# Kernel tuning notes

Measured on AMD Instinct MI355X. Metric: run time of the kernel, lower is better.

## Reference

```python
import jax, jax.numpy as jnp
import numpy as np

B, C, H, W = 8, 256, 64, 64
NH, FF, L, K = 8, 1024, 3, 64
THR = 0.5
DH = C // NH
SCALE = 1.0 / float(np.sqrt(DH))
N = H * W


def setup_inputs() -> dict:
    key = jax.random.key(0)
    ks = jax.random.split(key, 16)
    s = 0.02
    rn = lambda k, shape: (jax.random.normal(k, shape, jnp.float32) * s)
    return {
        "x": jax.random.normal(ks[0], (B, C, H, W), jnp.float32),
        "y": jax.random.normal(ks[1], (B, C, H, W), jnp.float32),
        "proj_w": rn(ks[2], (C, 2 * C)), "proj_b": rn(ks[3], (C,)),
        "sal_w": rn(ks[4], (1, C)), "sal_b": rn(ks[5], (1,)),
        "soft_w": rn(ks[6], (2, K, C)), "soft_b": rn(ks[7], (2, K)),
        "attn_in_w": rn(ks[8], (2, L, 3 * C, C)), "attn_in_b": rn(ks[9], (2, L, 3 * C)),
        "attn_out_w": rn(ks[10], (2, L, C, C)), "attn_out_b": rn(ks[11], (2, L, C)),
        "n1_g": jnp.ones((2, L, C), jnp.float32), "n1_b": jnp.zeros((2, L, C), jnp.float32),
        "ffn_w1": rn(ks[12], (2, L, FF, C)), "ffn_b1": rn(ks[13], (2, L, FF)),
        "ffn_w2": rn(ks[14], (2, L, C, FF)), "ffn_b2": rn(ks[15], (2, L, C)),
        "n2_g": jnp.ones((2, L, C), jnp.float32), "n2_b": jnp.zeros((2, L, C), jnp.float32),
    }


def _ln(t, g, b, eps=1e-5):
    m = t.mean(-1, keepdims=True)
    v = ((t - m) ** 2).mean(-1, keepdims=True)
    return (t - m) / jnp.sqrt(v + eps) * g + b


def _layers(q, kv, p, side):
    # q: [B,N,C] pixel queries, kv: [B,K,C] soft-pooled tokens
    for l in range(L):
        iw, ib = p["attn_in_w"][side, l], p["attn_in_b"][side, l]
        qq = (q @ iw[:C].T + ib[:C]).reshape(B, -1, NH, DH)
        kk = (kv @ iw[C:2 * C].T + ib[C:2 * C]).reshape(B, K, NH, DH)
        vv = (kv @ iw[2 * C:].T + ib[2 * C:]).reshape(B, K, NH, DH)
        att = jax.nn.softmax(jnp.einsum('bnhd,bkhd->bhnk', qq, kk) * SCALE, axis=-1)
        o = jnp.einsum('bhnk,bkhd->bnhd', att, vv).reshape(B, -1, C)
        o = o @ p["attn_out_w"][side, l].T + p["attn_out_b"][side, l]
        q = _ln(q + o, p["n1_g"][side, l], p["n1_b"][side, l])
        h = jax.nn.relu(q @ p["ffn_w1"][side, l].T + p["ffn_b1"][side, l])
        h = h @ p["ffn_w2"][side, l].T + p["ffn_b2"][side, l]
        q = _ln(q + h, p["n2_g"][side, l], p["n2_b"][side, l])
    return q


def _forward(x, y, proj_w, proj_b, sal_w, sal_b, soft_w, soft_b,
             attn_in_w, attn_in_b, attn_out_w, attn_out_b, n1_g, n1_b,
             ffn_w1, ffn_b1, ffn_w2, ffn_b2, n2_g, n2_b):
    p = dict(attn_in_w=attn_in_w, attn_in_b=attn_in_b, attn_out_w=attn_out_w,
             attn_out_b=attn_out_b, n1_g=n1_g, n1_b=n1_b, ffn_w1=ffn_w1,
             ffn_b1=ffn_b1, ffn_w2=ffn_w2, ffn_b2=ffn_b2, n2_g=n2_g, n2_b=n2_b)
    xc = jnp.concatenate([x, y], axis=1)                                  # [B,2C,H,W]
    feat = jnp.einsum('oc,bchw->bohw', proj_w, xc) + proj_b[None, :, None, None]
    sal = jnp.einsum('oc,bchw->bohw', sal_w, feat) + sal_b[None, :, None, None]  # [B,1,H,W]
    heat = jax.nn.sigmoid(sal)
    fg_mask = (heat >= THR).reshape(B, 1, N)
    bg_mask = (heat < 1.0 - THR).reshape(B, 1, N)
    fmap = feat.reshape(B, C, N)
    q0 = fmap.transpose(0, 2, 1)                                          # [B,N,C]
    out = fmap
    for side, hm in ((0, heat), (1, 1.0 - heat)):
        wf = feat * hm                                                    # [B,C,H,W]
        sw = (jnp.einsum('kc,bchw->bkhw', soft_w[side], wf)
              + soft_b[side][None, :, None, None]).reshape(B, K, N)       # [B,K,N]
        pool = jnp.einsum('bkn,bcn->bkc', sw, wf.reshape(B, C, N))        # [B,K,C]
        qs = _layers(q0, pool, p, side)                                   # [B,N,C]
        mask = fg_mask if side == 0 else bg_mask
        out = jnp.where(mask, qs.transpose(0, 2, 1), out)
    # per-image skip: if no fg or no bg pixels, keep original feature
    valid = fg_mask.any(axis=(1, 2)) & bg_mask.any(axis=(1, 2))           # [B]
    out = jnp.where(valid[:, None, None], out, fmap)
    return out.reshape(B, C, H, W)


def reference(x, y, proj_w, proj_b, sal_w, sal_b, soft_w, soft_b,
              attn_in_w, attn_in_b, attn_out_w, attn_out_b, n1_g, n1_b,
              ffn_w1, ffn_b1, ffn_w2, ffn_b2, n2_g, n2_b):
    return _forward(x, y, proj_w, proj_b, sal_w, sal_b, soft_w, soft_b,
                    attn_in_w, attn_in_b, attn_out_w, attn_out_b, n1_g, n1_b,
                    ffn_w1, ffn_b1, ffn_w2, ffn_b2, n2_g, n2_b)
```

## Files before the change

### kernel.cpp

```cpp
#include <hip/hip_runtime.h>
#include <stdint.h>

#define B_ 8
#define C_ 256
#define N_ 4096
#define K_ 64
#define NH_ 8
#define FF_ 1024
#define L_ 3
#define M_ (B_*N_)
#define SCALE_ 0.17677669529663687f

typedef float f32x4 __attribute__((ext_vector_type(4)));
typedef __bf16 v8bf __attribute__((ext_vector_type(8)));

__device__ __forceinline__ float b2f(unsigned short h){
  union { uint32_t u; float f; } v; v.u = ((uint32_t)h) << 16; return v.f;
}
__device__ __forceinline__ unsigned short f2b(float f){
  union { float f; uint32_t u; } v; v.f = f;
  uint32_t r = v.u + 0x7fffu + ((v.u >> 16) & 1u);
  return (unsigned short)(r >> 16);
}
__device__ __forceinline__ void gload_lds16(const void* g, void* l){
  __builtin_amdgcn_global_load_lds(
      (const __attribute__((address_space(1))) unsigned int*)g,
      (__attribute__((address_space(3))) unsigned int*)l, 16, 0, 0);
}

__global__ __launch_bounds__(256) void k_f32_to_bf16(const float* __restrict__ src,
                                                     unsigned short* __restrict__ dst, int n){
  int i4 = (blockIdx.x*256 + threadIdx.x)*4;
  if (i4 >= n) return;
  float4 v = *(const float4*)(src + i4);
  uint32_t p0 = (uint32_t)f2b(v.x) | ((uint32_t)f2b(v.y) << 16);
  uint32_t p1 = (uint32_t)f2b(v.z) | ((uint32_t)f2b(v.w) << 16);
  *(uint2*)(dst + i4) = make_uint2(p0, p1);
}

__global__ __launch_bounds__(256) void k_build_xcT(const float* __restrict__ x,
                                                   const float* __restrict__ y,
                                                   unsigned short* __restrict__ xcT){
  __shared__ float t[32][33];
  int b = blockIdx.z;
  int n0 = blockIdx.x*32, c0 = blockIdx.y*32;
  int tx = threadIdx.x, ty = threadIdx.y;
  const float* src = (c0 < 256) ? (x + ((size_t)b*256 + c0)*N_)
                                : (y + ((size_t)b*256 + (c0-256))*N_);
  #pragma unroll
  for (int i = 0; i < 4; i++){
    int cl = ty*4 + i;
    t[cl][tx] = src[(size_t)cl*N_ + n0 + tx];
  }
  __syncthreads();
  #pragma unroll
  for (int i = 0; i < 4; i++){
    int nl = ty*4 + i;
    xcT[((size_t)b*N_ + n0 + nl)*512 + c0 + tx] = f2b(t[tx][nl]);
  }
}

__global__ __launch_bounds__(256) void k_featmir(const float* __restrict__ featT,
                                                 unsigned short* __restrict__ featbf,
                                                 unsigned short* __restrict__ featC){
  __shared__ float t[32][33];
  int b = blockIdx.z;
  int n0 = blockIdx.x*32, c0 = blockIdx.y*32;
  int tx = threadIdx.x, ty = threadIdx.y;
  #pragma unroll
  for (int i = 0; i < 4; i++){
    int nl = ty*4 + i;
    size_t m = (size_t)b*N_ + n0 + nl;
    float v = featT[m*256 + c0 + tx];
    t[nl][tx] = v;
    featbf[m*256 + c0 + tx] = f2b(v);
  }
  __syncthreads();
  #pragma unroll
  for (int i = 0; i < 4; i++){
    int cl = ty*4 + i;
    featC[((size_t)b*256 + c0 + cl)*(size_t)N_ + n0 + tx] = f2b(t[tx][cl]);
  }
}

__global__ __launch_bounds__(512) void k_compute_u(const float* __restrict__ sal_w,
                                                   const float* __restrict__ proj_w,
                                                   const float* __restrict__ proj_b,
                                                   const float* __restrict__ sal_b,
                                                   double* __restrict__ u){
  int c2 = threadIdx.x;
  double acc = 0.0;
  for (int c = 0; c < 256; ++c)
    acc += (double)sal_w[c] * (double)proj_w[(size_t)c*512 + c2];
  u[c2] = acc;
  if (c2 == 0){
    double s0 = (double)sal_b[0];
    for (int c = 0; c < 256; ++c) s0 += (double)sal_w[c] * (double)proj_b[c];
    u[512] = s0;
  }
}

__global__ __launch_bounds__(256) void k_sal_part(const float* __restrict__ x,
                                                  const float* __restrict__ y,
                                                  const double* __restrict__ u,
                                                  double* __restrict__ part){
  int pix = blockIdx.x*256 + threadIdx.x;
  int cc = blockIdx.y;
  int b = pix >> 12, n = pix & 4095;
  int c0 = cc*32;
  const float* src = (c0 < 256) ? (x + ((size_t)b*256 + c0)*N_ + n)
                                : (y + ((size_t)b*256 + (c0-256))*N_ + n);
  const double* uu = u + c0;
  double acc = 0.0;
  #pragma unroll 8
  for (int c = 0; c < 32; ++c) acc += uu[c] * (double)src[(size_t)c*N_];
  part[(size_t)cc*32768 + pix] = acc;
}

__global__ __launch_bounds__(256) void k_sal_red(const double* __restrict__ part,
                                                 const double* __restrict__ u,
                                                 float* __restrict__ heat,
                                                 int* __restrict__ counts){
  int pix = blockIdx.x*256 + threadIdx.x;
  int b = pix >> 12;
  double acc = u[512];
  #pragma unroll
  for (int cc = 0; cc < 16; cc++) acc += part[(size_t)cc*32768 + pix];
  float hf = (float)(1.0 / (1.0 + exp(-acc)));
  heat[pix] = hf;
  unsigned long long mfg = __ballot(hf >= 0.5f);
  unsigned long long mbg = __ballot(hf < 0.5f);
  if ((threadIdx.x & 63) == 0){
    atomicAdd(&counts[b*2+0], (int)__popcll(mfg));
    atomicAdd(&counts[b*2+1], (int)__popcll(mbg));
  }
}

template<int EPI>
__global__ __launch_bounds__(256) void k_gemm_bt(
    const unsigned short* __restrict__ A, const unsigned short* __restrict__ W,
    const float* __restrict__ bias, void* __restrict__ out,
    int M, int N, int K){
  __shared__ unsigned short smem[2][2][128*64];
  int tid = threadIdx.x;
  int w = tid >> 6, l = tid & 63;
  int m0 = blockIdx.x * 128, n0 = blockIdx.y * 128;
  int wr = w >> 1, wc = w & 1;
  int lr = l & 15, lk = l >> 4;
  f32x4 acc[4][4] = {};
  int nt = K >> 6;
  #pragma unroll
  for (int i = 0; i < 4; i++){
    int idx = i*256 + tid;
    int row = idx >> 3, su = ((idx & 7) ^ (row & 7))*8;
    gload_lds16(A + (size_t)(m0+row)*K + su, &smem[0][0][idx*8]);
    gload_lds16(W + (size_t)(n0+row)*K + su, &smem[0][1][idx*8]);
  }
  __syncthreads();
  for (int t = 0; t < nt; ++t){
    int cur = t & 1;
    if (t + 1 < nt){
      int k0 = (t + 1) << 6;
      #pragma unroll
      for (int i = 0; i < 4; i++){
        int idx = i*256 + tid;
        int row = idx >> 3, su = ((idx & 7) ^ (row & 7))*8;
        gload_lds16(A + (size_t)(m0+row)*K + k0 + su, &smem[cur^1][0][idx*8]);
        gload_lds16(W + (size_t)(n0+row)*K + k0 + su, &smem[cur^1][1][idx*8]);
      }
    }
    const unsigned short* ldsA = smem[cur][0];
    const unsigned short* ldsB = smem[cur][1];
    #pragma unroll
    for (int kk = 0; kk < 2; kk++){
      v8bf af[4], bfr[4];
      #pragma unroll
      for (int f = 0; f < 4; f++){
        int ra = wr*64 + f*16 + lr;
        int rb2 = wc*64 + f*16 + lr;
        int u = kk*4 + lk;
        af[f]  = *(const v8bf*)(&ldsA[ra*64 + ((u ^ (ra&7))<<3)]);
        bfr[f] = *(const v8bf*)(&ldsB[rb2*64 + ((u ^ (rb2&7))<<3)]);
      }
      #pragma unroll
      for (int fi = 0; fi < 4; fi++)
        #pragma unroll
        for (int fj = 0; fj < 4; fj++)
          acc[fi][fj] = __builtin_amdgcn_mfma_f32_16x16x32_bf16(af[fi], bfr[fj], acc[fi][fj], 0, 0, 0);
    }
    __syncthreads();
  }
  if (EPI == 1 || EPI == 2){
    unsigned short* st = &smem[0][0][0];
    #pragma unroll
    for (int fj = 0; fj < 4; fj++){
      int col = wc*64 + fj*16 + lr;
      float bv = bias[n0 + col];
      #pragma unroll
      for (int fi = 0; fi < 4; fi++){
        int rl = wr*64 + fi*16 + lk*4;
        #pragma unroll
        for (int r = 0; r < 4; r++){
          float v = acc[fi][fj][r] + bv;
          if (EPI == 1) v = fmaxf(v, 0.f);
          st[(rl + r)*136 + col] = f2b(v);
        }
      }
    }
    __syncthreads();
    #pragma unroll
    for (int it = 0; it < 8; it++){
      int idx = it*256 + tid;
      int row = idx >> 4, c8 = (idx & 15)*8;
      *(uint4*)((unsigned short*)out + (size_t)(m0+row)*N + n0 + c8)
          = *(const uint4*)&st[row*136 + c8];
    }
  } else {
    #pragma unroll
    for (int fj = 0; fj < 4; fj++){
      int col = n0 + wc*64 + fj*16 + lr;
      float bv = bias[col];
      #pragma unroll
      for (int fi = 0; fi < 4; fi++){
        int rb = m0 + wr*64 + fi*16 + lk*4;
        #pragma unroll
        for (int r = 0; r < 4; r++){
          float v = acc[fi][fj][r] + bv;
          if (EPI == 3){
            int row = rb + r;
            ((unsigned short*)out)[((size_t)(row>>6)*256 + col)*64 + (row&63)] = f2b(v);
          } else {
            ((float*)out)[(size_t)(rb + r)*N + col] = v;
          }
        }
      }
    }
  }
}

__global__ __launch_bounds__(256) void k_kv(
    const unsigned short* __restrict__ pool, const unsigned short* __restrict__ iw,
    const float* __restrict__ ib, unsigned short* __restrict__ kk_bf,
    unsigned short* __restrict__ vvT_bf){
  __shared__ unsigned short smem[2][2][128*64];
  int tid = threadIdx.x;
  int w = tid >> 6, l = tid & 63;
  int m0 = blockIdx.x * 128, n0 = blockIdx.y * 128;
  int isv = blockIdx.z;
  const unsigned short* W = iw + (size_t)(isv ? 512 : 256)*256;
  const float* bias = ib + (isv ? 512 : 256);
  int wr = w >> 1, wc = w & 1;
  int lr = l & 15, lk = l >> 4;
  f32x4 acc[4][4] = {};
  #pragma unroll
  for (int i = 0; i < 4; i++){
    int idx = i*256 + tid;
    int row = idx >> 3, su = ((idx & 7) ^ (row & 7))*8;
    gload_lds16(pool + (size_t)(m0+row)*256 + su, &smem[0][0][idx*8]);
    gload_lds16(W + (size_t)(n0+row)*256 + su, &smem[0][1][idx*8]);
  }
  __syncthreads();
  for (int t = 0; t < 4; ++t){
    int cur = t & 1;
    if (t + 1 < 4){
      int k0 = (t + 1) << 6;
      #pragma unroll
      for (int i = 0; i < 4; i++){
        int idx = i*256 + tid;
        int row = idx >> 3, su = ((idx & 7) ^ (row & 7))*8;
        gload_lds16(pool + (size_t)(m0+row)*256 + k0 + su, &smem[cur^1][0][idx*8]);
        gload_lds16(W + (size_t)(n0+row)*256 + k0 + su, &smem[cur^1][1][idx*8]);
      }
    }
    const unsigned short* ldsA = smem[cur][0];
    const unsigned short* ldsB = smem[cur][1];
    #pragma unroll
    for (int kk = 0; kk < 2; kk++){
      v8bf af[4], bfr[4];
      #pragma unroll
      for (int f = 0; f < 4; f++){
        int ra = wr*64 + f*16 + lr;
        int rb2 = wc*64 + f*16 + lr;
        int u = kk*4 + lk;
        af[f]  = *(const v8bf*)(&ldsA[ra*64 + ((u ^ (ra&7))<<3)]);
        bfr[f] = *(const v8bf*)(&ldsB[rb2*64 + ((u ^ (rb2&7))<<3)]);
      }
      #pragma unroll
      for (int fi = 0; fi < 4; fi++)
        #pragma unroll
        for (int fj = 0; fj < 4; fj++)
          acc[fi][fj] = __builtin_amdgcn_mfma_f32_16x16x32_bf16(af[fi], bfr[fj], acc[fi][fj], 0, 0, 0);
    }
    __syncthreads();
  }
  #pragma unroll
  for (int fj = 0; fj < 4; fj++){
    int col = n0 + wc*64 + fj*16 + lr;
    float bv = bias[col];
    #pragma unroll
    for (int fi = 0; fi < 4; fi++){
      int rb = m0 + wr*64 + fi*16 + lk*4;
      #pragma unroll
      for (int r = 0; r < 4; r++){
        float v = acc[fi][fj][r] + bv;
        int row = rb + r;
        if (isv)
          vvT_bf[((size_t)(row>>6)*256 + col)*64 + (row&63)] = f2b(v);
        else
          kk_bf[(size_t)row*256 + col] = f2b(v);
      }
    }
  }
}

__global__ __launch_bounds__(512) void k_ffn(
    const unsigned short* __restrict__ qb, const unsigned short* __restrict__ W1g,
    const float* __restrict__ b1g, const unsigned short* __restrict__ W2g,
    const float* __restrict__ b2g, const float* __restrict__ n2g,
    const float* __restrict__ n2b, unsigned short* __restrict__ qout){
  __shared__ unsigned short smem[73728];
  unsigned short* sA  = smem;
  unsigned short* sW1 = smem + 32768;
  unsigned short* sW2 = smem + 49152;
  unsigned short* sH  = smem + 65536;
  int tid = threadIdx.x;
  int w = tid >> 6, l = tid & 63;
  int m0 = blockIdx.x * 128;
  int wm = w >> 2;
  int wf = w & 3;
  int lr = l & 15, lk = l >> 4;

  #pragma unroll
  for (int i = 0; i < 8; i++){
    int idx = i*512 + tid;
    int row = idx >> 5, g = idx & 31;
    int su = (g & 24) | ((g & 7) ^ (row & 7));
    gload_lds16(qb + (size_t)(m0+row)*256 + su*8, &sA[idx*8]);
  }
  #pragma unroll
  for (int i = 0; i < 4; i++){
    int idx = i*512 + tid;
    int row = idx >> 5, g = idx & 31;
    int su = (g & 24) | ((g & 7) ^ (row & 7));
    gload_lds16(W1g + (size_t)row*256 + su*8, &sW1[idx*8]);
  }
  #pragma unroll
  for (int i = 0; i < 4; i++){
    int idx = i*512 + tid;
    int row = idx >> 3, g = idx & 7;
    int su = g ^ (row & 7);
    gload_lds16(W2g + (size_t)row*1024 + su*8, &sW2[idx*8]);
  }
  __syncthreads();

  f32x4 acc[4][4] = {};
  for (int cc = 0; cc < 16; ++cc){
    f32x4 hacc[4] = {};
    #pragma unroll
    for (int ks = 0; ks < 8; ks++){
      int g = ks*4 + lk;
      int rf = wf*16 + lr;
      v8bf bf1 = *(const v8bf*)&sW1[rf*256 + (((g & 24) | ((g & 7) ^ (rf & 7)))<<3)];
      #pragma unroll
      for (int f = 0; f < 4; f++){
        int ra = wm*64 + f*16 + lr;
        v8bf af = *(const v8bf*)&sA[ra*256 + (((g & 24) | ((g & 7) ^ (ra & 7)))<<3)];
        hacc[f] = __builtin_amdgcn_mfma_f32_16x16x32_bf16(af, bf1, hacc[f], 0, 0, 0);
      }
    }
    {
      int fc = wf*16 + lr;
      float b1v = b1g[cc*64 + fc];
      #pragma unroll
      for (int fi = 0; fi < 4; fi++){
        int mr0 = wm*64 + fi*16 + lk*4;
        #pragma unroll
        for (int r = 0; r < 4; r++){
          float v = fmaxf(hacc[fi][r] + b1v, 0.f);
          int mr = mr0 + r;
          int key = (mr ^ (mr >> 3)) & 7;
          sH[mr*64 + (((fc >> 3) ^ key)<<3) + (fc & 7)] = f2b(v);
        }
      }
    }
    __syncthreads();
    if (cc + 1 < 16){
      int f0n = (cc+1)*64;
      #pragma unroll
      for (int i = 0; i < 4; i++){
        int idx = i*512 + tid;
        int row = idx >> 5, g = idx & 31;
        int su = (g & 24) | ((g & 7) ^ (row & 7));
        gload_lds16(W1g + (size_t)(f0n+row)*256 + su*8, &sW1[idx*8]);
      }
    }
    #pragma unroll
    for (int ks2 = 0; ks2 < 2; ks2++){
      int g = ks2*4 + lk;
      v8bf ha[4], wb[4];
      #pragma unroll
      for (int f = 0; f < 4; f++){
        int rh = wm*64 + f*16 + lr;
        int key = (rh ^ (rh >> 3)) & 7;
        ha[f] = *(const v8bf*)&sH[rh*64 + ((g ^ key)<<3)];
      }
      #pragma unroll
      for (int f = 0; f < 4; f++){
        int rc = wf*64 + f*16 + lr;
        wb[f] = *(const v8bf*)&sW2[rc*64 + ((g ^ (rc & 7))<<3)];
      }
      #pragma unroll
      for (int fi = 0; fi < 4; fi++)
        #pragma unroll
        for (int fc = 0; fc < 4; fc++)
          acc[fi][fc] = __builtin_amdgcn_mfma_f32_16x16x32_bf16(ha[fi], wb[fc], acc[fi][fc], 0, 0, 0);
    }
    __syncthreads();
    if (cc + 1 < 16){
      int f0n = (cc+1)*64;
      #pragma unroll
      for (int i = 0; i < 4; i++){
        int idx = i*512 + tid;
        int row = idx >> 3, g = idx & 7;
        int su = g ^ (row & 7);
        gload_lds16(W2g + (size_t)row*1024 + f0n + su*8, &sW2[idx*8]);
      }
    }
  }

  float b2v[4], gv[4], bev[4];
  #pragma unroll
  for (int fc = 0; fc < 4; fc++){
    int col = wf*64 + fc*16 + lr;
    b2v[fc] = b2g[col];
    gv[fc]  = n2g[col];
    bev[fc] = n2b[col];
  }
  #pragma unroll
  for (int fi = 0; fi < 4; fi++){
    #pragma unroll
    for (int r = 0; r < 4; r++){
      int row = wm*64 + fi*16 + lk*4 + r;
      #pragma unroll
      for (int fc = 0; fc < 4; fc++){
        int col = wf*64 + fc*16 + lr;
        int cu2 = col >> 3;
        int su = (cu2 & 24) | ((cu2 & 7) ^ (row & 7));
        float resid = b2f(sA[row*256 + su*8 + (col & 7)]);
        acc[fi][fc][r] += b2v[fc] + resid;
      }
    }
  }
  float* psum = (float*)(smem + 32768);
  float* psq  = psum + 512;
  float* mstd = psq + 512;
  #pragma unroll
  for (int fi = 0; fi < 4; fi++){
    #pragma unroll
    for (int r = 0; r < 4; r++){
      float s = acc[fi][0][r] + acc[fi][1][r] + acc[fi][2][r] + acc[fi][3][r];
      float q = acc[fi][0][r]*acc[fi][0][r] + acc[fi][1][r]*acc[fi][1][r]
              + acc[fi][2][r]*acc[fi][2][r] + acc[fi][3][r]*acc[fi][3][r];
      s += __shfl_xor(s, 1); s += __shfl_xor(s, 2);
      s += __shfl_xor(s, 4); s += __shfl_xor(s, 8);
      q += __shfl_xor(q, 1); q += __shfl_xor(q, 2);
      q += __shfl_xor(q, 4); q += __shfl_xor(q, 8);
      if (lr == 0){
        int row = wm*64 + fi*16 + lk*4 + r;
        psum[row*4 + wf] = s;
        psq[row*4 + wf]  = q;
      }
    }
  }
  __syncthreads();
  if (tid < 128){
    float s = psum[tid*4] + psum[tid*4+1] + psum[tid*4+2] + psum[tid*4+3];
    float q = psq[tid*4] + psq[tid*4+1] + psq[tid*4+2] + psq[tid*4+3];
    float mean = s * (1.0f/256.0f);
    float var = q * (1.0f/256.0f) - mean*mean;
    mstd[tid*2]   = mean;
    mstd[tid*2+1] = 1.0f / sqrtf(var + 1e-5f);
  }
  __syncthreads();
  unsigned short* st = smem;
  #pragma unroll
  for (int fi = 0; fi < 4; fi++){
    #pragma unroll
    for (int r = 0; r < 4; r++){
      int rowl = wm*64 + fi*16 + lk*4 + r;
      float mean = mstd[rowl*2], rstd = mstd[rowl*2+1];
      #pragma unroll
      for (int fc = 0; fc < 4; fc++){
        int col = wf*64 + fc*16 + lr;
        st[rowl*264 + col] = f2b((acc[fi][fc][r] - mean)*rstd*gv[fc] + bev[fc]);
      }
    }
  }
  __syncthreads();
  #pragma unroll
  for (int it = 0; it < 8; it++){
    int idx = it*512 + tid;
    int row = idx >> 5, c8 = (idx & 31)*8;
    *(uint4*)(qout + (size_t)(m0+row)*256 + c8) = *(const uint4*)&st[row*264 + c8];
  }
}

__global__ __launch_bounds__(256) void k_swh(const float* __restrict__ g_all,
                                             const float* __restrict__ heat,
                                             const float* __restrict__ soft_b,
                                             unsigned short* __restrict__ swh){
  __shared__ float gl[64*129];
  __shared__ float hml[64];
  int tid = threadIdx.x;
  int blk = blockIdx.x;
  size_t m0 = (size_t)blk*64;
  int b = (int)(m0 >> 12), n0 = (int)(m0 & 4095);
  #pragma unroll
  for (int i = 0; i < 32; i++){
    int idx = i*256 + tid;
    int row = idx >> 7, col = idx & 127;
    gl[row*129 + col] = g_all[(m0 + row)*128 + col];
  }
  if (tid < 64) hml[tid] = heat[(size_t)b*4096 + n0 + tid];
  __syncthreads();
  int k = tid >> 2, j0 = (tid & 3)*16;
  #pragma unroll
  for (int s = 0; s < 2; s++){
    float sb = soft_b[s*64 + k];
    unsigned short vals[16];
    #pragma unroll
    for (int j = 0; j < 16; j++){
      int n = j0 + j;
      float h = hml[n];
      float hm = s ? (1.0f - h) : h;
      vals[j] = f2b((gl[n*129 + s*64 + k]*hm + sb)*hm);
    }
    unsigned short* dst = swh + (((size_t)b*2 + s)*64 + k)*4096 + n0 + j0;
    uint4 o0, o1;
    o0.x = vals[0] | ((uint32_t)vals[1]<<16);  o0.y = vals[2] | ((uint32_t)vals[3]<<16);
    o0.z = vals[4] | ((uint32_t)vals[5]<<16);  o0.w = vals[6] | ((uint32_t)vals[7]<<16);
    o1.x = vals[8] | ((uint32_t)vals[9]<<16);  o1.y = vals[10]| ((uint32_t)vals[11]<<16);
    o1.z = vals[12]| ((uint32_t)vals[13]<<16); o1.w = vals[14]| ((uint32_t)vals[15]<<16);
    *(uint4*)dst = o0;
    *(uint4*)(dst + 8) = o1;
  }
}

__global__ __launch_bounds__(256) void k_poolgemm(
    const unsigned short* __restrict__ swh, const unsigned short* __restrict__ featC,
    float* __restrict__ pp){
  __shared__ unsigned short ldsA[128*64];
  __shared__ unsigned short ldsB[128*64];
  int tid = threadIdx.x;
  int w = tid >> 6, l = tid & 63;
  int kc = blockIdx.x, nt = blockIdx.y, b = blockIdx.z;
  int wr = w >> 1, wc = w & 1;
  int lr = l & 15, lk = l >> 4;
  const unsigned short* A = swh  + (size_t)b*128*4096 + kc*512;
  const unsigned short* W = featC + ((size_t)b*256 + nt*128)*4096 + kc*512;
  f32x4 acc[4][4] = {};
  for (int k0 = 0; k0 < 512; k0 += 64){
    #pragma unroll
    for (int i = 0; i < 4; i++){
      int idx = i*256 + tid;
      int row = idx >> 3, su = (idx & 7) ^ (row & 7);
      gload_lds16(A + (size_t)row*4096 + k0 + su*8, &ldsA[idx*8]);
    }
    #pragma unroll
    for (int i = 0; i < 4; i++){
      int idx = i*256 + tid;
      int row = idx >> 3, su = (idx & 7) ^ (row & 7);
      gload_lds16(W + (size_t)row*4096 + k0 + su*8, &ldsB[idx*8]);
    }
    __syncthreads();
    #pragma unroll
    for (int kk = 0; kk < 2; kk++){
      v8bf af[4], bfr[4];
      #pragma unroll
      for (int f = 0; f < 4; f++){
        int ra = wr*64 + f*16 + lr;
        int rb2 = wc*64 + f*16 + lr;
        int u = kk*4 + lk;
        af[f]  = *(const v8bf*)(&ldsA[ra*64 + ((u ^ (ra&7))<<3)]);
        bfr[f] = *(const v8bf*)(&ldsB[rb2*64 + ((u ^ (rb2&7))<<3)]);
      }
      #pragma unroll
      for (int fi = 0; fi < 4; fi++)
        #pragma unroll
        for (int fj = 0; fj < 4; fj++)
          acc[fi][fj] = __builtin_amdgcn_mfma_f32_16x16x32_bf16(af[fi], bfr[fj], acc[fi][fj], 0, 0, 0);
    }
    __syncthreads();
  }
  float* dst = pp + ((size_t)kc*8 + b)*128*256;
  #pragma unroll
  for (int fj = 0; fj < 4; fj++){
    int col = nt*128 + wc*64 + fj*16 + lr;
    #pragma unroll
    for (int fi = 0; fi < 4; fi++){
      int rb = wr*64 + fi*16 + lk*4;
      #pragma unroll
      for (int r = 0; r < 4; r++)
        dst[(size_t)(rb + r)*256 + col] = acc[fi][fj][r];
    }
  }
}

__global__ __launch_bounds__(256) void k_pool2b(const float* __restrict__ pp,
                                                unsigned short* __restrict__ pool_bf_s){
  int bk = blockIdx.x, side = blockIdx.y, c = threadIdx.x;
  int b = bk >> 6, k = bk & 63;
  float s = 0.f;
  #pragma unroll
  for (int kc = 0; kc < 8; kc++)
    s += pp[(((size_t)kc*8 + b)*128 + side*64 + k)*256 + c];
  pool_bf_s[((size_t)side*512 + bk)*256 + c] = f2b(s);
}

__global__ __launch_bounds__(256) void k_attn2(
    const unsigned short* __restrict__ qq, const unsigned short* __restrict__ kk,
    const unsigned short* __restrict__ vvT, unsigned short* __restrict__ obf){
  __shared__ unsigned short sk[64*256];
  __shared__ unsigned short svT[256*64];
  __shared__ unsigned short sp[4][16*64];
  __shared__ unsigned short sow[4][16*32];
  int tid = threadIdx.x, w = tid >> 6, l = tid & 63;
  int blk = blockIdx.x, b = blk >> 6;
  int l15 = l & 15, lg = l >> 4;
  const uint4* ksrc = (const uint4*)(kk + (size_t)b*64*256);
  #pragma unroll
  for (int i = 0; i < 8; i++){
    int u = i*256 + tid;
    int row = u >> 5, j = u & 31;
    *(uint4*)&sk[row*256 + ((j ^ (row&7))<<3)] = ksrc[u];
  }
  const uint4* vsrc = (const uint4*)(vvT + (size_t)b*256*64);
  #pragma unroll
  for (int i = 0; i < 8; i++){
    int u = i*256 + tid;
    int row = u >> 3, j = u & 7;
    *(uint4*)&svT[row*64 + ((j ^ (row&7))<<3)] = vsrc[u];
  }
  __syncthreads();
  size_t qrow = (size_t)blk*64 + w*16 + l15;
  for (int h = 0; h < 8; h++){
    v8bf aq = *(const v8bf*)(qq + qrow*256 + h*32 + lg*8);
    f32x4 s[4];
    #pragma unroll
    for (int kt = 0; kt < 4; kt++){
      int row = kt*16 + l15;
      v8bf bk = *(const v8bf*)&sk[row*256 + (((h*4 + lg) ^ (row&7))<<3)];
      f32x4 z = {};
      s[kt] = __builtin_amdgcn_mfma_f32_16x16x32_bf16(aq, bk, z, 0, 0, 0);
    }
    #pragma unroll
    for (int r = 0; r < 4; r++){
      float v0 = s[0][r]*SCALE_, v1 = s[1][r]*SCALE_;
      float v2 = s[2][r]*SCALE_, v3 = s[3][r]*SCALE_;
      float mx = fmaxf(fmaxf(v0, v1), fmaxf(v2, v3));
      mx = fmaxf(mx, __shfl_xor(mx, 1));
      mx = fmaxf(mx, __shfl_xor(mx, 2));
      mx = fmaxf(mx, __shfl_xor(mx, 4));
      mx = fmaxf(mx, __shfl_xor(mx, 8));
      float e0 = __expf(v0-mx), e1 = __expf(v1-mx);
      float e2 = __expf(v2-mx), e3 = __expf(v3-mx);
      float sum = e0+e1+e2+e3;
      sum += __shfl_xor(sum, 1); sum += __shfl_xor(sum, 2);
      sum += __shfl_xor(sum, 4); sum += __shfl_xor(sum, 8);
      float inv = 1.0f/sum;
      s[0][r] = e0*inv; s[1][r] = e1*inv; s[2][r] = e2*inv; s[3][r] = e3*inv;
    }
    #pragma unroll
    for (int kt = 0; kt < 4; kt++){
      int colu = kt*2 + (l15>>3);
      #pragma unroll
      for (int r = 0; r < 4; r++){
        int row = lg*4 + r;
        sp[w][row*64 + ((colu ^ (row&7))<<3) + (l&7)] = f2b(s[kt][r]);
      }
    }
    f32x4 o[2] = {};
    #pragma unroll
    for (int k2 = 0; k2 < 2; k2++){
      v8bf pa = *(const v8bf*)&sp[w][l15*64 + (((k2*4 + lg) ^ (l15&7))<<3)];
      #pragma unroll
      for (int dt = 0; dt < 2; dt++){
        int vrow = h*32 + dt*16 + l15;
        v8bf bv = *(const v8bf*)&svT[vrow*64 + (((k2*4 + lg) ^ (vrow&7))<<3)];
        o[dt] = __builtin_amdgcn_mfma_f32_16x16x32_bf16(pa, bv, o[dt], 0, 0, 0);
      }
    }
    #pragma unroll
    for (int dt = 0; dt < 2; dt++)
      #pragma unroll
      for (int r = 0; r < 4; r++)
        sow[w][(lg*4 + r)*32 + dt*16 + l15] = f2b(o[dt][r]);
    uint4 ov = *(const uint4*)&sow[w][l15*32 + lg*8];
    *(uint4*)(obf + qrow*256 + h*32 + lg*8) = ov;
  }
}

template<int RF32>
__global__ __launch_bounds__(256) void k_ln2(
    const void* __restrict__ resid, const unsigned short* __restrict__ delta,
    const float* __restrict__ g, const float* __restrict__ bta,
    unsigned short* __restrict__ qout){
  int wv = threadIdx.x >> 6, l = threadIdx.x & 63;
  size_t m = (size_t)blockIdx.x*4 + wv;
  uint2 dv = *(const uint2*)(delta + m*256 + l*4);
  float d0 = b2f((unsigned short)(dv.x & 0xffff)), d1 = b2f((unsigned short)(dv.x >> 16));
  float d2 = b2f((unsigned short)(dv.y & 0xffff)), d3 = b2f((unsigned short)(dv.y >> 16));
  float x0, x1, x2, x3;
  if (RF32){
    float4 rv = *(const float4*)((const float*)resid + m*256 + l*4);
    x0 = rv.x+d0; x1 = rv.y+d1; x2 = rv.z+d2; x3 = rv.w+d3;
  } else {
    uint2 rv = *(const uint2*)((const unsigned short*)resid + m*256 + l*4);
    x0 = b2f((unsigned short)(rv.x & 0xffff)) + d0;
    x1 = b2f((unsigned short)(rv.x >> 16)) + d1;
    x2 = b2f((unsigned short)(rv.y & 0xffff)) + d2;
    x3 = b2f((unsigned short)(rv.y >> 16)) + d3;
  }
  float s = x0+x1+x2+x3;
  float ss = x0*x0+x1*x1+x2*x2+x3*x3;
  #pragma unroll
  for (int off = 32; off; off >>= 1){
    s  += __shfl_xor(s, off);
    ss += __shfl_xor(ss, off);
  }
  float mean = s * (1.0f/256.0f);
  float var = ss * (1.0f/256.0f) - mean*mean;
  float rstd = 1.0f / sqrtf(var + 1e-5f);
  float4 gv = *(const float4*)(g + l*4);
  float4 bv = *(const float4*)(bta + l*4);
  float y0 = (x0-mean)*rstd*gv.x + bv.x;
  float y1 = (x1-mean)*rstd*gv.y + bv.y;
  float y2 = (x2-mean)*rstd*gv.z + bv.z;
  float y3 = (x3-mean)*rstd*gv.w + bv.w;
  uint32_t p0 = (uint32_t)f2b(y0) | ((uint32_t)f2b(y1)<<16);
  uint32_t p1 = (uint32_t)f2b(y2) | ((uint32_t)f2b(y3)<<16);
  *(uint2*)(qout + m*256 + l*4) = make_uint2(p0,p1);
}

__global__ __launch_bounds__(256) void k_select(
    const unsigned short* __restrict__ qA, const unsigned short* __restrict__ qB,
    const float* __restrict__ featT, const float* __restrict__ heat,
    const int* __restrict__ counts, float* __restrict__ out){
  __shared__ float t[32][33];
  int b = blockIdx.z;
  int n0 = blockIdx.x*32, c0 = blockIdx.y*32;
  int tx = threadIdx.x, ty = threadIdx.y;
  bool valid = (counts[b*2] > 0) && (counts[b*2+1] > 0);
  #pragma unroll
  for (int i = 0; i < 4; i++){
    int nl = ty*4+i;
    size_t m = (size_t)b*4096 + n0 + nl;
    float v;
    if (!valid) v = featT[m*256 + c0 + tx];
    else {
      bool fg = heat[(size_t)b*4096 + n0 + nl] >= 0.5f;
      v = fg ? b2f(qA[m*256 + c0 + tx]) : b2f(qB[m*256 + c0 + tx]);
    }
    t[nl][tx] = v;
  }
  __syncthreads();
  #pragma unroll
  for (int i = 0; i < 4; i++){
    int cl = ty*4+i;
    out[((size_t)b*256 + c0 + cl)*4096 + n0 + tx] = t[tx][cl];
  }
}

extern "C" void kernel_launch(void* const* d_in, const int* in_sizes, int n_in,
                              void* d_out, int out_size, void* d_ws, size_t ws_size,
                              hipStream_t stream){
  const float* x         = (const float*)d_in[0];
  const float* y         = (const float*)d_in[1];
  const float* proj_w    = (const float*)d_in[2];
  const float* proj_b    = (const float*)d_in[3];
  const float* sal_w     = (const float*)d_in[4];
  const float* sal_b     = (const float*)d_in[5];
  const float* soft_w    = (const float*)d_in[6];
  const float* soft_b    = (const float*)d_in[7];
  const float* attn_in_w = (const float*)d_in[8];
  const float* attn_in_b = (const float*)d_in[9];
  const float* attn_out_w= (const float*)d_in[10];
  const float* attn_out_b= (const float*)d_in[11];
  const float* n1_g      = (const float*)d_in[12];
  const float* n1_b      = (const float*)d_in[13];
  const float* ffn_w1    = (const float*)d_in[14];
  const float* ffn_b1    = (const float*)d_in[15];
  const float* ffn_w2    = (const float*)d_in[16];
  const float* ffn_b2    = (const float*)d_in[17];
  const float* n2_g      = (const float*)d_in[18];
  const float* n2_b      = (const float*)d_in[19];
  float* out = (float*)d_out;

  char* p = (char*)d_ws;
  auto alloc = [&](size_t bytes){ char* r = p; p += (bytes + 255) & ~(size_t)255; return r; };
  unsigned short* hbf   = (unsigned short*)alloc((size_t)M_*FF_*2);
  unsigned short* xcT   = hbf;
  unsigned short* qq_bf = hbf;
  float* featT = (float*)alloc((size_t)M_*C_*4);
  unsigned short* qAb = (unsigned short*)alloc((size_t)M_*C_*2);
  unsigned short* swh = qAb;
  unsigned short* qBb = (unsigned short*)alloc((size_t)M_*C_*2);
  unsigned short* obf = (unsigned short*)alloc((size_t)M_*C_*2);
  unsigned short* featC = obf;
  unsigned short* featbf = (unsigned short*)alloc((size_t)M_*C_*2);
  unsigned short* tmpb = (unsigned short*)alloc((size_t)M_*C_*2);
  float* g_all = (float*)tmpb;
  float* pp    = (float*)alloc((size_t)8*8*128*256*4);
  double* salp = (double*)pp;
  unsigned short* pool_bf_s = (unsigned short*)alloc((size_t)2*512*256*2);
  unsigned short* kk_bf = (unsigned short*)alloc((size_t)B_*K_*C_*2);
  unsigned short* vvT_bf= (unsigned short*)alloc((size_t)B_*C_*K_*2);
  float* heat = (float*)alloc((size_t)B_*N_*4);
  double* u   = (double*)alloc(513*8);
  int* counts = (int*)alloc(64);
  float* zbias = (float*)alloc(512);
  unsigned short* projw_bf = (unsigned short*)alloc((size_t)C_*512*2);
  unsigned short* aiw_bf = (unsigned short*)alloc((size_t)2*L_*768*C_*2);
  unsigned short* aow_bf = (unsigned short*)alloc((size_t)2*L_*C_*C_*2);
  unsigned short* f1w_bf = (unsigned short*)alloc((size_t)2*L_*FF_*C_*2);
  unsigned short* f2w_bf = (unsigned short*)alloc((size_t)2*L_*C_*FF_*2);
  unsigned short* sw2_bf = (unsigned short*)alloc((size_t)2*K_*C_*2);

  hipMemsetAsync(counts, 0, 64, stream);
  hipMemsetAsync(zbias, 0, 512, stream);
  k_compute_u<<<1, 512, 0, stream>>>(sal_w, proj_w, proj_b, sal_b, u);
  k_sal_part<<<dim3(128, 16), 256, 0, stream>>>(x, y, u, salp);
  k_sal_red<<<128, 256, 0, stream>>>(salp, u, heat, counts);

  auto conv = [&](const float* s, unsigned short* d, size_t n){
    k_f32_to_bf16<<<(unsigned)((n/4 + 255)/256), 256, 0, stream>>>(s, d, (int)n);
  };
  conv(proj_w,     projw_bf, (size_t)C_*512);
  conv(attn_in_w,  aiw_bf,   (size_t)2*L_*768*C_);
  conv(attn_out_w, aow_bf,   (size_t)2*L_*C_*C_);
  conv(ffn_w1,     f1w_bf,   (size_t)2*L_*FF_*C_);
  conv(ffn_w2,     f2w_bf,   (size_t)2*L_*C_*FF_);
  conv(soft_w,     sw2_bf,   (size_t)2*K_*C_);

  k_build_xcT<<<dim3(N_/32, 512/32, B_), dim3(32,8), 0, stream>>>(x, y, xcT);
  k_gemm_bt<0><<<dim3(M_/128, C_/128), 256, 0, stream>>>(xcT, projw_bf, proj_b, featT, M_, C_, 512);
  k_featmir<<<dim3(N_/32, C_/32, B_), dim3(32,8), 0, stream>>>(featT, featbf, featC);

  k_gemm_bt<0><<<dim3(M_/128, 1), 256, 0, stream>>>(featbf, sw2_bf, zbias, g_all, M_, 128, C_);
  k_swh<<<M_/64, 256, 0, stream>>>(g_all, heat, soft_b, swh);
  k_poolgemm<<<dim3(8, 2, B_), 256, 0, stream>>>(swh, featC, pp);
  k_pool2b<<<dim3(512, 2), 256, 0, stream>>>(pp, pool_bf_s);

  for (int side = 0; side < 2; ++side){
    unsigned short* qb = side ? qBb : qAb;
    const unsigned short* poolS = pool_bf_s + (size_t)side*512*256;
    for (int lyr = 0; lyr < L_; ++lyr){
      int sl = side*L_ + lyr;
      const unsigned short* iw = aiw_bf + (size_t)sl*768*C_;
      const float* ib = attn_in_b + (size_t)sl*768;
      const unsigned short* qin = (lyr == 0) ? featbf : qb;
      k_gemm_bt<2><<<dim3(M_/128, C_/128), 256, 0, stream>>>(qin, iw, ib, qq_bf, M_, C_, C_);
      k_kv<<<dim3(4, 2, 2), 256, 0, stream>>>(poolS, iw, ib, kk_bf, vvT_bf);
      k_attn2<<<M_/64, 256, 0, stream>>>(qq_bf, kk_bf, vvT_bf, obf);
      k_gemm_bt<2><<<dim3(M_/128, C_/128), 256, 0, stream>>>(obf, aow_bf + (size_t)sl*C_*C_, attn_out_b + (size_t)sl*C_, tmpb, M_, C_, C_);
      if (lyr == 0)
        k_ln2<1><<<M_/4, 256, 0, stream>>>(featT, tmpb, n1_g + (size_t)sl*C_, n1_b + (size_t)sl*C_, qb);
      else
        k_ln2<0><<<M_/4, 256, 0, stream>>>(qb, tmpb, n1_g + (size_t)sl*C_, n1_b + (size_t)sl*C_, qb);
      k_ffn<<<M_/128, 512, 0, stream>>>(qb, f1w_bf + (size_t)sl*FF_*C_, ffn_b1 + (size_t)sl*FF_,
                                        f2w_bf + (size_t)sl*C_*FF_, ffn_b2 + (size_t)sl*C_,
                                        n2_g + (size_t)sl*C_, n2_b + (size_t)sl*C_, qb);
    }
  }
  k_select<<<dim3(N_/32, C_/32, B_), dim3(32,8), 0, stream>>>(qAb, qBb, featT, heat, counts, out);
}
```

Baseline: 822.6 us.

## Fuse attention output projection with residual add and LayerNorm

Replaces the separate output-projection GEMM and LayerNorm kernel with one kernel that computes a full 128x256 row tile, double-buffers the K slices in LDS, then adds bias and residual and applies LayerNorm per row before writing bf16. This removes the round trip of the intermediate tensor through global memory and one launch per layer. The FFN epilogue is also reworked to stage the GEMM output in LDS and compute LayerNorm with four threads per row instead of cross-wave partial sums. The new kernel uses 512 threads and more registers per thread, which may lower occupancy.

```diff
diff --git a/kernel.cpp b/kernel.cpp
--- a/kernel.cpp
+++ b/kernel.cpp
@@ -26,6 +26,12 @@
   __builtin_amdgcn_global_load_lds(
       (const __attribute__((address_space(1))) unsigned int*)g,
       (__attribute__((address_space(3))) unsigned int*)l, 16, 0, 0);
+}
+__device__ __forceinline__ void unpack8(uint4 v, float* o){
+  o[0]=b2f((unsigned short)(v.x & 0xffff)); o[1]=b2f((unsigned short)(v.x >> 16));
+  o[2]=b2f((unsigned short)(v.y & 0xffff)); o[3]=b2f((unsigned short)(v.y >> 16));
+  o[4]=b2f((unsigned short)(v.z & 0xffff)); o[5]=b2f((unsigned short)(v.z >> 16));
+  o[6]=b2f((unsigned short)(v.w & 0xffff)); o[7]=b2f((unsigned short)(v.w >> 16));
 }
 
 __global__ __launch_bounds__(256) void k_f32_to_bf16(const float* __restrict__ src,
@@ -313,6 +319,141 @@
   }
 }
 
+template<int RF32>
+__global__ __launch_bounds__(512) void k_gemm_ln(
+    const unsigned short* __restrict__ A, const unsigned short* __restrict__ W,
+    const float* __restrict__ bias, const void* __restrict__ resid,
+    const float* __restrict__ g, const float* __restrict__ bta,
+    unsigned short* __restrict__ qout){
+  __shared__ unsigned short smem[49152];
+  int tid = threadIdx.x;
+  int w = tid >> 6, l = tid & 63;
+  int m0 = blockIdx.x * 128;
+  int wm = w >> 2, wf = w & 3;
+  int lr = l & 15, lk = l >> 4;
+  f32x4 acc[4][4] = {};
+  #pragma unroll
+  for (int i = 0; i < 2; i++){
+    int idx = i*512 + tid;
+    int row = idx >> 3, su = ((idx & 7) ^ (row & 7))*8;
+    gload_lds16(A + (size_t)(m0+row)*256 + su, &smem[idx*8]);
+  }
+  #pragma unroll
+  for (int i = 0; i < 4; i++){
+    int idx = i*512 + tid;
+    int row = idx >> 3, su = ((idx & 7) ^ (row & 7))*8;
+    gload_lds16(W + (size_t)row*256 + su, &smem[8192 + idx*8]);
+  }
+  __syncthreads();
+  for (int t = 0; t < 4; ++t){
+    int cur = t & 1;
+    if (t + 1 < 4){
+      int k0 = (t + 1) << 6;
+      unsigned short* bA = smem + (cur^1)*24576;
+      unsigned short* bB = bA + 8192;
+      #pragma unroll
+      for (int i = 0; i < 2; i++){
+        int idx = i*512 + tid;
+        int row = idx >> 3, su = ((idx & 7) ^ (row & 7))*8;
+        gload_lds16(A + (size_t)(m0+row)*256 + k0 + su, &bA[idx*8]);
+      }
+      #pragma unroll
+      for (int i = 0; i < 4; i++){
+        int idx = i*512 + tid;
+        int row = idx >> 3, su = ((idx & 7) ^ (row & 7))*8;
+        gload_lds16(W + (size_t)row*256 + k0 + su, &bB[idx*8]);
+      }
+    }
+    const unsigned short* bA = smem + cur*24576;
+    const unsigned short* bB = bA + 8192;
+    #pragma unroll
+    for (int kk = 0; kk < 2; kk++){
+      v8bf af[4], wb[4];
+      int u = kk*4 + lk;
+      #pragma unroll
+      for (int f = 0; f < 4; f++){
+        int ra = wm*64 + f*16 + lr;
+        af[f] = *(const v8bf*)&bA[ra*64 + ((u ^ (ra&7))<<3)];
+      }
+      #pragma unroll
+      for (int f = 0; f < 4; f++){
+        int rc = wf*64 + f*16 + lr;
+        wb[f] = *(const v8bf*)&bB[rc*64 + ((u ^ (rc&7))<<3)];
+      }
+      #pragma unroll
+      for (int fi = 0; fi < 4; fi++)
+        #pragma unroll
+        for (int fc = 0; fc < 4; fc++)
+          acc[fi][fc] = __builtin_amdgcn_mfma_f32_16x16x32_bf16(af[fi], wb[fc], acc[fi][fc], 0, 0, 0);
+    }
+    __syncthreads();
+  }
+  unsigned short* st = smem;
+  #pragma unroll
+  for (int fc = 0; fc < 4; fc++){
+    int col = wf*64 + fc*16 + lr;
+    float bv = bias[col];
+    #pragma unroll
+    for (int fi = 0; fi < 4; fi++){
+      int rl = wm*64 + fi*16 + lk*4;
+      #pragma unroll
+      for (int r = 0; r < 4; r++)
+        st[(rl + r)*264 + col] = f2b(acc[fi][fc][r] + bv);
+    }
+  }
+  __syncthreads();
+  int row = tid >> 2, seg = tid & 3;
+  float xv[64];
+  #pragma unroll
+  for (int j = 0; j < 8; j++){
+    int cu = seg*8 + j;
+    uint4 dv = *(const uint4*)&st[row*264 + cu*8];
+    float dd[8];
+    unpack8(dv, dd);
+    if (RF32){
+      const float* rp = (const float*)resid + (size_t)(m0+row)*256 + cu*8;
+      float4 r0 = *(const float4*)rp, r1 = *(const float4*)(rp + 4);
+      xv[j*8+0] = r0.x + dd[0]; xv[j*8+1] = r0.y + dd[1];
+      xv[j*8+2] = r0.z + dd[2]; xv[j*8+3] = r0.w + dd[3];
+      xv[j*8+4] = r1.x + dd[4]; xv[j*8+5] = r1.y + dd[5];
+      xv[j*8+6] = r1.z + dd[6]; xv[j*8+7] = r1.w + dd[7];
+    } else {
+      uint4 rv = *(const uint4*)((const unsigned short*)resid + (size_t)(m0+row)*256 + cu*8);
+      float rr[8];
+      unpack8(rv, rr);
+      #pragma unroll
+      for (int e = 0; e < 8; e++) xv[j*8+e] = rr[e] + dd[e];
+    }
+  }
+  float s = 0.f, q = 0.f;
+  #pragma unroll
+  for (int i2 = 0; i2 < 64; i2++){ s += xv[i2]; q += xv[i2]*xv[i2]; }
+  s += __shfl_xor(s, 1); s += __shfl_xor(s, 2);
+  q += __shfl_xor(q, 1); q += __shfl_xor(q, 2);
+  float mean = s * (1.0f/256.0f);
+  float rstd = 1.0f / sqrtf(q*(1.0f/256.0f) - mean*mean + 1e-5f);
+  #pragma unroll
+  for (int j = 0; j < 8; j++){
+    int c0 = seg*64 + j*8;
+    float4 g0 = *(const float4*)(g + c0), g1 = *(const float4*)(g + c0 + 4);
+    float4 b0 = *(const float4*)(bta + c0), b1 = *(const float4*)(bta + c0 + 4);
+    float y0 = (xv[j*8+0]-mean)*rstd*g0.x + b0.x;
+    float y1 = (xv[j*8+1]-mean)*rstd*g0.y + b0.y;
+    float y2 = (xv[j*8+2]-mean)*rstd*g0.z + b0.z;
+    float y3 = (xv[j*8+3]-mean)*rstd*g0.w + b0.w;
+    float y4 = (xv[j*8+4]-mean)*rstd*g1.x + b1.x;
+    float y5 = (xv[j*8+5]-mean)*rstd*g1.y + b1.y;
+    float y6 = (xv[j*8+6]-mean)*rstd*g1.z + b1.z;
+    float y7 = (xv[j*8+7]-mean)*rstd*g1.w + b1.w;
+    uint4 ov;
+    ov.x = (uint32_t)f2b(y0) | ((uint32_t)f2b(y1)<<16);
+    ov.y = (uint32_t)f2b(y2) | ((uint32_t)f2b(y3)<<16);
+    ov.z = (uint32_t)f2b(y4) | ((uint32_t)f2b(y5)<<16);
+    ov.w = (uint32_t)f2b(y6) | ((uint32_t)f2b(y7)<<16);
+    *(uint4*)(qout + (size_t)(m0+row)*256 + c0) = ov;
+  }
+}
+
 __global__ __launch_bounds__(512) void k_ffn(
     const unsigned short* __restrict__ qb, const unsigned short* __restrict__ W1g,
     const float* __restrict__ b1g, const unsigned short* __restrict__ W2g,
@@ -326,29 +467,28 @@
   int tid = threadIdx.x;
   int w = tid >> 6, l = tid & 63;
   int m0 = blockIdx.x * 128;
-  int wm = w >> 2;
-  int wf = w & 3;
+  int wm = w >> 2, wf = w & 3;
   int lr = l & 15, lk = l >> 4;
 
   #pragma unroll
   for (int i = 0; i < 8; i++){
     int idx = i*512 + tid;
-    int row = idx >> 5, g = idx & 31;
-    int su = (g & 24) | ((g & 7) ^ (row & 7));
+    int row = idx >> 5, gu = idx & 31;
+    int su = (gu & 24) | ((gu & 7) ^ (row & 7));
     gload_lds16(qb + (size_t)(m0+row)*256 + su*8, &sA[idx*8]);
   }
   #pragma unroll
   for (int i = 0; i < 4; i++){
     int idx = i*512 + tid;
-    int row = idx >> 5, g = idx & 31;
-    int su = (g & 24) | ((g & 7) ^ (row & 7));
+    int row = idx >> 5, gu = idx & 31;
+    int su = (gu & 24) | ((gu & 7) ^ (row & 7));
     gload_lds16(W1g + (size_t)row*256 + su*8, &sW1[idx*8]);
   }
   #pragma unroll
   for (int i = 0; i < 4; i++){
     int idx = i*512 + tid;
-    int row = idx >> 3, g = idx & 7;
-    int su = g ^ (row & 7);
+    int row = idx >> 3, gu = idx & 7;
+    int su = gu ^ (row & 7);
     gload_lds16(W2g + (size_t)row*1024 + su*8, &sW2[idx*8]);
   }
   __syncthreads();
@@ -358,13 +498,13 @@
     f32x4 hacc[4] = {};
     #pragma unroll
     for (int ks = 0; ks < 8; ks++){
-      int g = ks*4 + lk;
+      int gu = ks*4 + lk;
       int rf = wf*16 + lr;
-      v8bf bf1 = *(const v8bf*)&sW1[rf*256 + (((g & 24) | ((g & 7) ^ (rf & 7)))<<3)];
+      v8bf bf1 = *(const v8bf*)&sW1[rf*256 + (((gu & 24) | ((gu & 7) ^ (rf & 7)))<<3)];
       #pragma unroll
       for (int f = 0; f < 4; f++){
         int ra = wm*64 + f*16 + lr;
-        v8bf af = *(const v8bf*)&sA[ra*256 + (((g & 24) | ((g & 7) ^ (ra & 7)))<<3)];
+        v8bf af = *(const v8bf*)&sA[ra*256 + (((gu & 24) | ((gu & 7) ^ (ra & 7)))<<3)];
         hacc[f] = __builtin_amdgcn_mfma_f32_16x16x32_bf16(af, bf1, hacc[f], 0, 0, 0);
       }
     }
@@ -389,25 +529,25 @@
       #pragma unroll
       for (int i = 0; i < 4; i++){
         int idx = i*512 + tid;
-        int row = idx >> 5, g = idx & 31;
-        int su = (g & 24) | ((g & 7) ^ (row & 7));
+        int row = idx >> 5, gu = idx & 31;
+        int su = (gu & 24) | ((gu & 7) ^ (row & 7));
         gload_lds16(W1g + (size_t)(f0n+row)*256 + su*8, &sW1[idx*8]);
       }
     }
     #pragma unroll
     for (int ks2 = 0; ks2 < 2; ks2++){
-      int g = ks2*4 + lk;
+      int gu = ks2*4 + lk;
       v8bf ha[4], wb[4];
       #pragma unroll
       for (int f = 0; f < 4; f++){
         int rh = wm*64 + f*16 + lr;
         int key = (rh ^ (rh >> 3)) & 7;
-        ha[f] = *(const v8bf*)&sH[rh*64 + ((g ^ key)<<3)];
+        ha[f] = *(const v8bf*)&sH[rh*64 + ((gu ^ key)<<3)];
       }
       #pragma unroll
       for (int f = 0; f < 4; f++){
         int rc = wf*64 + f*16 + lr;
-        wb[f] = *(const v8bf*)&sW2[rc*64 + ((g ^ (rc & 7))<<3)];
+        wb[f] = *(const v8bf*)&sW2[rc*64 + ((gu ^ (rc & 7))<<3)];
       }
       #pragma unroll
       for (int fi = 0; fi < 4; fi++)
@@ -421,87 +561,66 @@
       #pragma unroll
       for (int i = 0; i < 4; i++){
         int idx = i*512 + tid;
-        int row = idx >> 3, g = idx & 7;
-        int su = g ^ (row & 7);
+        int row = idx >> 3, gu = idx & 7;
+        int su = gu ^ (row & 7);
         gload_lds16(W2g + (size_t)row*1024 + f0n + su*8, &sW2[idx*8]);
       }
     }
   }
 
-  float b2v[4], gv[4], bev[4];
+  unsigned short* st = smem + 32768;
   #pragma unroll
   for (int fc = 0; fc < 4; fc++){
     int col = wf*64 + fc*16 + lr;
-    b2v[fc] = b2g[col];
-    gv[fc]  = n2g[col];
-    bev[fc] = n2b[col];
-  }
-  #pragma unroll
-  for (int fi = 0; fi < 4; fi++){
-    #pragma unroll
-    for (int r = 0; r < 4; r++){
-      int row = wm*64 + fi*16 + lk*4 + r;
-      #pragma unroll
-      for (int fc = 0; fc < 4; fc++){
-        int col = wf*64 + fc*16 + lr;
-        int cu2 = col >> 3;
-        int su = (cu2 & 24) | ((cu2 & 7) ^ (row & 7));
-        float resid = b2f(sA[row*256 + su*8 + (col & 7)]);
-        acc[fi][fc][r] += b2v[fc] + resid;
-      }
-    }
-  }
-  float* psum = (float*)(smem + 32768);
-  float* psq  = psum + 512;
-  float* mstd = psq + 512;
-  #pragma unroll
-  for (int fi = 0; fi < 4; fi++){
-    #pragma unroll
-    for (int r = 0; r < 4; r++){
-      float s = acc[fi][0][r] + acc[fi][1][r] + acc[fi][2][r] + acc[fi][3][r];
-      float q = acc[fi][0][r]*acc[fi][0][r] + acc[fi][1][r]*acc[fi][1][r]
-              + acc[fi][2][r]*acc[fi][2][r] + acc[fi][3][r]*acc[fi][3][r];
-      s += __shfl_xor(s, 1); s += __shfl_xor(s, 2);
-      s += __shfl_xor(s, 4); s += __shfl_xor(s, 8);
-      q += __shfl_xor(q, 1); q += __shfl_xor(q, 2);
-      q += __shfl_xor(q, 4); q += __shfl_xor(q, 8);
-      if (lr == 0){
-        int row = wm*64 + fi*16 + lk*4 + r;
-        psum[row*4 + wf] = s;
-        psq[row*4 + wf]  = q;
-      }
-    }
-  }
-  __syncthreads();
-  if (tid < 128){
-    float s = psum[tid*4] + psum[tid*4+1] + psum[tid*4+2] + psum[tid*4+3];
-    float q = psq[tid*4] + psq[tid*4+1] + psq[tid*4+2] + psq[tid*4+3];
-    float mean = s * (1.0f/256.0f);
-    float var = q * (1.0f/256.0f) - mean*mean;
-    mstd[tid*2]   = mean;
-    mstd[tid*2+1] = 1.0f / sqrtf(var + 1e-5f);
-  }
-  __syncthreads();
-  unsigned short* st = smem;
-  #pragma unroll
-  for (int fi = 0; fi < 4; fi++){
-    #pragma unroll
-    for (int r = 0; r < 4; r++){
-      int rowl = wm*64 + fi*16 + lk*4 + r;
-      float mean = mstd[rowl*2], rstd = mstd[rowl*2+1];
-      #pragma unroll
-      for (int fc = 0; fc < 4; fc++){
-        int col = wf*64 + fc*16 + lr;
-        st[rowl*264 + col] = f2b((acc[fi][fc][r] - mean)*rstd*gv[fc] + bev[fc]);
-      }
-    }
-  }
-  __syncthreads();
-  #pragma unroll
-  for (int it = 0; it < 8; it++){
-    int idx = it*512 + tid;
-    int row = idx >> 5, c8 = (idx & 31)*8;
-    *(uint4*)(qout + (size_t)(m0+row)*256 + c8) = *(const uint4*)&st[row*264 + c8];
+    float bv = b2g[col];
+    #pragma unroll
+    for (int fi = 0; fi < 4; fi++){
+      int rl = wm*64 + fi*16 + lk*4;
+      #pragma unroll
+      for (int r = 0; r < 4; r++)
+        st[(rl + r)*264 + col] = f2b(acc[fi][fc][r] + bv);
+    }
+  }
+  __syncthreads();
+  int row = tid >> 2, seg = tid & 3;
+  float xv[64];
+  #pragma unroll
+  for (int j = 0; j < 8; j++){
+    int cu = seg*8 + j;
+    int su = (cu & 24) | ((cu & 7) ^ (row & 7));
+    uint4 rv = *(const uint4*)&sA[row*256 + su*8];
+    uint4 dv = *(const uint4*)&st[row*264 + cu*8];
+    float rr[8], dd[8];
+    unpack8(rv, rr); unpack8(dv, dd);
+    #pragma unroll
+    for (int e = 0; e < 8; e++) xv[j*8+e] = rr[e] + dd[e];
+  }
+  float s = 0.f, q = 0.f;
+  #pragma unroll
+  for (int i2 = 0; i2 < 64; i2++){ s += xv[i2]; q += xv[i2]*xv[i2]; }
+  s += __shfl_xor(s, 1); s += __shfl_xor(s, 2);
+  q += __shfl_xor(q, 1); q += __shfl_xor(q, 2);
+  float mean = s * (1.0f/256.0f);
+  float rstd = 1.0f / sqrtf(q*(1.0f/256.0f) - mean*mean + 1e-5f);
+  #pragma unroll
+  for (int j = 0; j < 8; j++){
+    int c0 = seg*64 + j*8;
+    float4 g0 = *(const float4*)(n2g + c0), g1 = *(const float4*)(n2g + c0 + 4);
+    float4 b0 = *(const float4*)(n2b + c0), b1 = *(const float4*)(n2b + c0 + 4);
+    float y0 = (xv[j*8+0]-mean)*rstd*g0.x + b0.x;
+    float y1 = (xv[j*8+1]-mean)*rstd*g0.y + b0.y;
+    float y2 = (xv[j*8+2]-mean)*rstd*g0.z + b0.z;
+    float y3 = (xv[j*8+3]-mean)*rstd*g0.w + b0.w;
+    float y4 = (xv[j*8+4]-mean)*rstd*g1.x + b1.x;
+    float y5 = (xv[j*8+5]-mean)*rstd*g1.y + b1.y;
+    float y6 = (xv[j*8+6]-mean)*rstd*g1.z + b1.z;
+    float y7 = (xv[j*8+7]-mean)*rstd*g1.w + b1.w;
+    uint4 ov;
+    ov.x = (uint32_t)f2b(y0) | ((uint32_t)f2b(y1)<<16);
+    ov.y = (uint32_t)f2b(y2) | ((uint32_t)f2b(y3)<<16);
+    ov.z = (uint32_t)f2b(y4) | ((uint32_t)f2b(y5)<<16);
+    ov.w = (uint32_t)f2b(y6) | ((uint32_t)f2b(y7)<<16);
+    *(uint4*)(qout + (size_t)(m0+row)*256 + c0) = ov;
   }
 }
 
@@ -698,48 +817,6 @@
     uint4 ov = *(const uint4*)&sow[w][l15*32 + lg*8];
     *(uint4*)(obf + qrow*256 + h*32 + lg*8) = ov;
   }
-}
-
-template<int RF32>
-__global__ __launch_bounds__(256) void k_ln2(
-    const void* __restrict__ resid, const unsigned short* __restrict__ delta,
-    const float* __restrict__ g, const float* __restrict__ bta,
-    unsigned short* __restrict__ qout){
-  int wv = threadIdx.x >> 6, l = threadIdx.x & 63;
-  size_t m = (size_t)blockIdx.x*4 + wv;
-  uint2 dv = *(const uint2*)(delta + m*256 + l*4);
-  float d0 = b2f((unsigned short)(dv.x & 0xffff)), d1 = b2f((unsigned short)(dv.x >> 16));
-  float d2 = b2f((unsigned short)(dv.y & 0xffff)), d3 = b2f((unsigned short)(dv.y >> 16));
-  float x0, x1, x2, x3;
-  if (RF32){
-    float4 rv = *(const float4*)((const float*)resid + m*256 + l*4);
-    x0 = rv.x+d0; x1 = rv.y+d1; x2 = rv.z+d2; x3 = rv.w+d3;
-  } else {
-    uint2 rv = *(const uint2*)((const unsigned short*)resid + m*256 + l*4);
-    x0 = b2f((unsigned short)(rv.x & 0xffff)) + d0;
-    x1 = b2f((unsigned short)(rv.x >> 16)) + d1;
-    x2 = b2f((unsigned short)(rv.y & 0xffff)) + d2;
-    x3 = b2f((unsigned short)(rv.y >> 16)) + d3;
-  }
-  float s = x0+x1+x2+x3;
-  float ss = x0*x0+x1*x1+x2*x2+x3*x3;
-  #pragma unroll
-  for (int off = 32; off; off >>= 1){
-    s  += __shfl_xor(s, off);
-    ss += __shfl_xor(ss, off);
-  }
-  float mean = s * (1.0f/256.0f);
-  float var = ss * (1.0f/256.0f) - mean*mean;
-  float rstd = 1.0f / sqrtf(var + 1e-5f);
-  float4 gv = *(const float4*)(g + l*4);
-  float4 bv = *(const float4*)(bta + l*4);
-  float y0 = (x0-mean)*rstd*gv.x + bv.x;
-  float y1 = (x1-mean)*rstd*gv.y + bv.y;
-  float y2 = (x2-mean)*rstd*gv.z + bv.z;
-  float y3 = (x3-mean)*rstd*gv.w + bv.w;
-  uint32_t p0 = (uint32_t)f2b(y0) | ((uint32_t)f2b(y1)<<16);
-  uint32_t p1 = (uint32_t)f2b(y2) | ((uint32_t)f2b(y3)<<16);
-  *(uint2*)(qout + m*256 + l*4) = make_uint2(p0,p1);
 }
 
 __global__ __launch_bounds__(256) void k_select(
@@ -862,11 +939,12 @@
       k_gemm_bt<2><<<dim3(M_/128, C_/128), 256, 0, stream>>>(qin, iw, ib, qq_bf, M_, C_, C_);
       k_kv<<<dim3(4, 2, 2), 256, 0, stream>>>(poolS, iw, ib, kk_bf, vvT_bf);
       k_attn2<<<M_/64, 256, 0, stream>>>(qq_bf, kk_bf, vvT_bf, obf);
-      k_gemm_bt<2><<<dim3(M_/128, C_/128), 256, 0, stream>>>(obf, aow_bf + (size_t)sl*C_*C_, attn_out_b + (size_t)sl*C_, tmpb, M_, C_, C_);
       if (lyr == 0)
-        k_ln2<1><<<M_/4, 256, 0, stream>>>(featT, tmpb, n1_g + (size_t)sl*C_, n1_b + (size_t)sl*C_, qb);
+        k_gemm_ln<1><<<M_/128, 512, 0, stream>>>(obf, aow_bf + (size_t)sl*C_*C_,
+            attn_out_b + (size_t)sl*C_, featT, n1_g + (size_t)sl*C_, n1_b + (size_t)sl*C_, qb);
       else
-        k_ln2<0><<<M_/4, 256, 0, stream>>>(qb, tmpb, n1_g + (size_t)sl*C_, n1_b + (size_t)sl*C_, qb);
+        k_gemm_ln<0><<<M_/128, 512, 0, stream>>>(obf, aow_bf + (size_t)sl*C_*C_,
+            attn_out_b + (size_t)sl*C_, qb, n1_g + (size_t)sl*C_, n1_b + (size_t)sl*C_, qb);
       k_ffn<<<M_/128, 512, 0, stream>>>(qb, f1w_bf + (size_t)sl*FF_*C_, ffn_b1 + (size_t)sl*FF_,
                                         f2w_bf + (size_t)sl*C_*FF_, ffn_b2 + (size_t)sl*C_,
                                         n2_g + (size_t)sl*C_, n2_b + (size_t)sl*C_, qb);
```

Measured after the change: 917.9 us. 1.12x slower.
